# Kernel optimization log

Measured on AMD Instinct MI355X. Metric: run time of the kernel, lower is better.

The kernel has to match this reference:

```python
import jax, jax.numpy as jnp
import numpy as np

C, B, F, O, DK = 10, 8192, 256, 64, 5


def setup_inputs() -> dict:
    key = jax.random.key(0)
    ks = jax.random.split(key, 7)
    x = jax.random.normal(ks[0], (B, F), jnp.float32)
    y = jax.random.normal(ks[1], (B, C), jnp.float32)
    # kaiming-uniform-like init scales
    w_key = jax.random.normal(ks[2], (C, 1, 1, DK), jnp.float32) * 0.5
    w_query = jax.random.normal(ks[3], (C, 1, DK), jnp.float32) * 0.5
    w_value = jax.random.normal(ks[4], (C, 1, 1), jnp.float32) * 0.5
    weight = jax.random.normal(ks[5], (C, 1, F, O), jnp.float32) * (1.0 / np.sqrt(F))
    bias = jax.random.normal(ks[6], (C, 1, O), jnp.float32) * 0.1
    return {"x": x, "y": y, "w_key": w_key, "w_query": w_query,
            "w_value": w_value, "weight": weight, "bias": bias}


def reference(x, y, w_key, w_query, w_value, weight, bias):
    # x: [B,F] (first=True -> conceptually [1,B,F]); y: [B,C]
    yt = y.T                                             # [C,B]
    querys = yt[..., None] * w_query                     # [C,B,1]*[C,1,DK] -> [C,B,DK]
    # keys[c,b,f,k] = x[b,f] * w_key[c,k]; attn_scores[c,b,f] = sum_k keys*querys
    #              = x[b,f] * (w_key[c] . querys[c,b])  (rank-1 structure, fused)
    kq = jnp.einsum('ck,cbk->cb', w_key.reshape(w_key.shape[0], -1), querys)  # [C,B]
    # mean over batch dim, then softmax over features
    scores_avg = jnp.einsum('bf,cb->cf', x, kq) / x.shape[0]  # [C,F]
    sm = jax.nn.softmax(scores_avg, axis=-1)                  # [C,F]
    attn = sm / jnp.max(sm, axis=-1, keepdims=True)           # [C,F] max-normalized
    values = x[None, :, :] * w_value                          # [1,B,F]*[C,1,1] -> [C,B,F]
    weighted = values * attn[:, None, :]                      # [C,B,F]
    # (weighted[...,None,:] @ weight).squeeze() + bias -> [C,B,O]
    out = jnp.einsum('cbf,cfo->cbo', weighted, weight[:, 0]) + bias  # bias [C,1,O]
    return out
```

## Files before the change

### kernel.cpp

```cpp
#include <hip/hip_runtime.h>
#include <hip/hip_bf16.h>

#define C_ 10
#define B_ 8192
#define F_ 256
#define O_ 64
#define DK_ 5
#define NBLK1 256
#define NG2   16

typedef __attribute__((ext_vector_type(8))) short short8;
typedef __attribute__((ext_vector_type(4))) float floatx4;

static __device__ __forceinline__ unsigned short f2bf(float f) {
    union { float f; unsigned u; } v; v.f = f;
    unsigned r = v.u + 0x7fffu + ((v.u >> 16) & 1u);
    return (unsigned short)(r >> 16);
}

__global__ __launch_bounds__(256) void k1_reduce(const float* __restrict__ x,
                                                 const float* __restrict__ y,
                                                 float* __restrict__ G_part,
                                                 unsigned short* __restrict__ xb) {
    __shared__ float xl[32 * F_];
    __shared__ float yl[32 * C_];
    const int b0 = blockIdx.x * 32;
    const int t  = threadIdx.x;

    for (int i = t; i < 32 * C_; i += 256) yl[i] = y[b0 * C_ + i];

    const int r  = t >> 6;
    const int f4 = (t & 63) * 4;
#pragma unroll
    for (int j = 0; j < 8; ++j) {
        int row = r + 4 * j;
        float4 v = *(const float4*)(x + (size_t)(b0 + row) * F_ + f4);
        *(float4*)(xl + row * F_ + f4) = v;
        ushort4 s;
        s.x = f2bf(v.x); s.y = f2bf(v.y); s.z = f2bf(v.z); s.w = f2bf(v.w);
        *(ushort4*)(xb + (size_t)(b0 + row) * F_ + f4) = s;
    }
    __syncthreads();

    float acc[C_];
#pragma unroll
    for (int c = 0; c < C_; ++c) acc[c] = 0.f;

#pragma unroll 8
    for (int b = 0; b < 32; ++b) {
        float xv = xl[b * F_ + t];
#pragma unroll
        for (int c = 0; c < C_; ++c) acc[c] = fmaf(yl[b * C_ + c], xv, acc[c]);
    }

    float* gp = G_part + (size_t)blockIdx.x * C_ * F_ + t;
#pragma unroll
    for (int c = 0; c < C_; ++c) gp[c * F_] = acc[c];
}

__global__ __launch_bounds__(256) void k1b_reduce(const float* __restrict__ G_part,
                                                  float* __restrict__ G2) {
    const int c = (int)blockIdx.x >> 4;
    const int g = (int)blockIdx.x & 15;
    const int t = threadIdx.x;
    const float* gp = G_part + (size_t)(g * 16) * C_ * F_ + c * F_ + t;
    float a0 = 0.f, a1 = 0.f, a2 = 0.f, a3 = 0.f;
#pragma unroll
    for (int i = 0; i < 16; i += 4) {
        a0 += gp[(size_t)(i + 0) * C_ * F_];
        a1 += gp[(size_t)(i + 1) * C_ * F_];
        a2 += gp[(size_t)(i + 2) * C_ * F_];
        a3 += gp[(size_t)(i + 3) * C_ * F_];
    }
    G2[(size_t)g * C_ * F_ + c * F_ + t] = (a0 + a1) + (a2 + a3);
}

__global__ __launch_bounds__(256) void k2_wprep(const float* __restrict__ G2,
                                                const float* __restrict__ w_key,
                                                const float* __restrict__ w_query,
                                                const float* __restrict__ w_value,
                                                const float* __restrict__ weight,
                                                unsigned short* __restrict__ WT) {
    __shared__ float a2[F_];
    __shared__ float wred[4];
    const int c    = blockIdx.x >> 2;
    const int part = blockIdx.x & 3;
    const int t    = threadIdx.x;

    const float* gp = G2 + c * F_ + t;
    float g0 = 0.f, g1 = 0.f, g2 = 0.f, g3 = 0.f;
#pragma unroll
    for (int i = 0; i < NG2; i += 4) {
        g0 += gp[(size_t)(i + 0) * C_ * F_];
        g1 += gp[(size_t)(i + 1) * C_ * F_];
        g2 += gp[(size_t)(i + 2) * C_ * F_];
        g3 += gp[(size_t)(i + 3) * C_ * F_];
    }
    float g = (g0 + g1) + (g2 + g3);

    float s = 0.f;
#pragma unroll
    for (int k = 0; k < DK_; ++k) s += w_key[c * DK_ + k] * w_query[c * DK_ + k];

    float z = s * g * (1.0f / (float)B_);
    float m = z;
#pragma unroll
    for (int off = 32; off >= 1; off >>= 1) m = fmaxf(m, __shfl_xor(m, off));
    if ((t & 63) == 0) wred[t >> 6] = m;
    __syncthreads();
    float mm = fmaxf(fmaxf(wred[0], wred[1]), fmaxf(wred[2], wred[3]));
    a2[t] = expf(z - mm) * w_value[c];
    __syncthreads();

    const int o  = t & 63;
    const int fg = t >> 6;
    const float* wsrc = weight + (size_t)c * F_ * O_;
    char* wdst = (char*)(WT + (size_t)c * O_ * F_);
#pragma unroll
    for (int gi = 0; gi < 2; ++gi) {
        int f0 = part * 64 + fg * 16 + gi * 8;
        short8 v8;
#pragma unroll
        for (int e = 0; e < 8; ++e) {
            int f = f0 + e;
            v8[e] = (short)f2bf(wsrc[f * O_ + o] * a2[f]);
        }
        int byte = o * 512 + ((2 * f0) ^ ((o & 7) << 4));
        *(short8*)(wdst + byte) = v8;
    }
}

__global__ __launch_bounds__(256) void k3_mfma(const unsigned short* __restrict__ xb,
                                               const unsigned short* __restrict__ WT,
                                               const float* __restrict__ bias,
                                               float* __restrict__ out) {
    __shared__ unsigned short wt[O_ * F_];
    const int c  = blockIdx.y;
    const int b0 = blockIdx.x * 64;
    const int t  = threadIdx.x;
    const int w  = t >> 6;
    const int l  = t & 63;
    const int lr = l & 15;
    const int lg = l >> 4;

    const unsigned short* xrow = xb + (size_t)(b0 + w * 16 + lr) * F_;
    short8 a[8];
#pragma unroll
    for (int k0 = 0; k0 < 8; ++k0) a[k0] = *(const short8*)(xrow + k0 * 32 + lg * 8);

    {
        const short8* src = (const short8*)(WT + (size_t)c * O_ * F_);
        short8* dst = (short8*)wt;
#pragma unroll
        for (int j = 0; j < 8; ++j) dst[t + 256 * j] = src[t + 256 * j];
    }
    __syncthreads();

    floatx4 acc[4];
#pragma unroll
    for (int n = 0; n < 4; ++n) {
        float bo = bias[c * O_ + n * 16 + lr];
        acc[n] = (floatx4){bo, bo, bo, bo};
    }

#pragma unroll
    for (int k0 = 0; k0 < 8; ++k0) {
#pragma unroll
        for (int n = 0; n < 4; ++n) {
            int o = n * 16 + lr;
            int byte = o * 512 + ((k0 * 64 + lg * 16) ^ ((o & 7) << 4));
            short8 bf = *(const short8*)((const char*)wt + byte);
            acc[n] = __builtin_amdgcn_mfma_f32_16x16x32_bf16(a[k0], bf, acc[n], 0, 0, 0);
        }
    }

#pragma unroll
    for (int n = 0; n < 4; ++n) {
        int col = n * 16 + lr;
#pragma unroll
        for (int r = 0; r < 4; ++r) {
            int row = b0 + w * 16 + lg * 4 + r;
            out[((size_t)c * B_ + row) * O_ + col] = acc[n][r];
        }
    }
}

extern "C" void kernel_launch(void* const* d_in, const int* in_sizes, int n_in,
                              void* d_out, int out_size, void* d_ws, size_t ws_size,
                              hipStream_t stream) {
    const float* x       = (const float*)d_in[0];
    const float* y       = (const float*)d_in[1];
    const float* w_key   = (const float*)d_in[2];
    const float* w_query = (const float*)d_in[3];
    const float* w_value = (const float*)d_in[4];
    const float* weight  = (const float*)d_in[5];
    const float* bias    = (const float*)d_in[6];
    float* out = (float*)d_out;

    char* ws = (char*)d_ws;
    unsigned short* xb     = (unsigned short*)ws;
    unsigned short* WT     = (unsigned short*)(ws + (size_t)B_ * F_ * 2);
    float*          G_part = (float*)(ws + (size_t)B_ * F_ * 2 + C_ * O_ * F_ * 2);
    float*          G2     = G_part + (size_t)NBLK1 * C_ * F_;

    k1_reduce<<<NBLK1, 256, 0, stream>>>(x, y, G_part, xb);
    k1b_reduce<<<C_ * NG2, 256, 0, stream>>>(G_part, G2);
    k2_wprep<<<C_ * 4, 256, 0, stream>>>(G2, w_key, w_query, w_value, weight, WT);
    dim3 g3(B_ / 64, C_);
    k3_mfma<<<g3, 256, 0, stream>>>(xb, WT, bias, out);
}
```

Before: 27.72 us.

## Fuse weight preparation into the MFMA kernel, recomputing it per block

Removes the separate weight-prep kernel and its global bf16 WT buffer. Each GEMM block now reduces G2 itself, computes the softmax-derived scaling, scales and converts the 64KB fp32 weight slice, and writes it swizzled into shared memory. This saves one kernel launch and a global round trip. In exchange, all 1280 blocks redo the softmax and weight conversion and read the fp32 weights, which are twice the size of the bf16 copy they used to read.

```diff
diff --git a/kernel.cpp b/kernel.cpp
--- a/kernel.cpp
+++ b/kernel.cpp
@@ -75,66 +75,17 @@
     G2[(size_t)g * C_ * F_ + c * F_ + t] = (a0 + a1) + (a2 + a3);
 }
 
-__global__ __launch_bounds__(256) void k2_wprep(const float* __restrict__ G2,
+__global__ __launch_bounds__(256) void k3_fused(const unsigned short* __restrict__ xb,
+                                                const float* __restrict__ G2,
                                                 const float* __restrict__ w_key,
                                                 const float* __restrict__ w_query,
                                                 const float* __restrict__ w_value,
                                                 const float* __restrict__ weight,
-                                                unsigned short* __restrict__ WT) {
+                                                const float* __restrict__ bias,
+                                                float* __restrict__ out) {
+    __shared__ unsigned short wt[O_ * F_];
     __shared__ float a2[F_];
     __shared__ float wred[4];
-    const int c    = blockIdx.x >> 2;
-    const int part = blockIdx.x & 3;
-    const int t    = threadIdx.x;
-
-    const float* gp = G2 + c * F_ + t;
-    float g0 = 0.f, g1 = 0.f, g2 = 0.f, g3 = 0.f;
-#pragma unroll
-    for (int i = 0; i < NG2; i += 4) {
-        g0 += gp[(size_t)(i + 0) * C_ * F_];
-        g1 += gp[(size_t)(i + 1) * C_ * F_];
-        g2 += gp[(size_t)(i + 2) * C_ * F_];
-        g3 += gp[(size_t)(i + 3) * C_ * F_];
-    }
-    float g = (g0 + g1) + (g2 + g3);
-
-    float s = 0.f;
-#pragma unroll
-    for (int k = 0; k < DK_; ++k) s += w_key[c * DK_ + k] * w_query[c * DK_ + k];
-
-    float z = s * g * (1.0f / (float)B_);
-    float m = z;
-#pragma unroll
-    for (int off = 32; off >= 1; off >>= 1) m = fmaxf(m, __shfl_xor(m, off));
-    if ((t & 63) == 0) wred[t >> 6] = m;
-    __syncthreads();
-    float mm = fmaxf(fmaxf(wred[0], wred[1]), fmaxf(wred[2], wred[3]));
-    a2[t] = expf(z - mm) * w_value[c];
-    __syncthreads();
-
-    const int o  = t & 63;
-    const int fg = t >> 6;
-    const float* wsrc = weight + (size_t)c * F_ * O_;
-    char* wdst = (char*)(WT + (size_t)c * O_ * F_);
-#pragma unroll
-    for (int gi = 0; gi < 2; ++gi) {
-        int f0 = part * 64 + fg * 16 + gi * 8;
-        short8 v8;
-#pragma unroll
-        for (int e = 0; e < 8; ++e) {
-            int f = f0 + e;
-            v8[e] = (short)f2bf(wsrc[f * O_ + o] * a2[f]);
-        }
-        int byte = o * 512 + ((2 * f0) ^ ((o & 7) << 4));
-        *(short8*)(wdst + byte) = v8;
-    }
-}
-
-__global__ __launch_bounds__(256) void k3_mfma(const unsigned short* __restrict__ xb,
-                                               const unsigned short* __restrict__ WT,
-                                               const float* __restrict__ bias,
-                                               float* __restrict__ out) {
-    __shared__ unsigned short wt[O_ * F_];
     const int c  = blockIdx.y;
     const int b0 = blockIdx.x * 64;
     const int t  = threadIdx.x;
@@ -149,10 +100,46 @@
     for (int k0 = 0; k0 < 8; ++k0) a[k0] = *(const short8*)(xrow + k0 * 32 + lg * 8);
 
     {
-        const short8* src = (const short8*)(WT + (size_t)c * O_ * F_);
-        short8* dst = (short8*)wt;
+        const float* gp = G2 + c * F_ + t;
+        float g0 = 0.f, g1 = 0.f, g2 = 0.f, g3 = 0.f;
 #pragma unroll
-        for (int j = 0; j < 8; ++j) dst[t + 256 * j] = src[t + 256 * j];
+        for (int i = 0; i < NG2; i += 4) {
+            g0 += gp[(size_t)(i + 0) * C_ * F_];
+            g1 += gp[(size_t)(i + 1) * C_ * F_];
+            g2 += gp[(size_t)(i + 2) * C_ * F_];
+            g3 += gp[(size_t)(i + 3) * C_ * F_];
+        }
+        float g = (g0 + g1) + (g2 + g3);
+
+        float s = 0.f;
+#pragma unroll
+        for (int k = 0; k < DK_; ++k) s += w_key[c * DK_ + k] * w_query[c * DK_ + k];
+
+        float z = s * g * (1.0f / (float)B_);
+        float m = z;
+#pragma unroll
+        for (int off = 32; off >= 1; off >>= 1) m = fmaxf(m, __shfl_xor(m, off));
+        if ((t & 63) == 0) wred[t >> 6] = m;
+        __syncthreads();
+        float mm = fmaxf(fmaxf(wred[0], wred[1]), fmaxf(wred[2], wred[3]));
+        a2[t] = expf(z - mm) * w_value[c];
+        __syncthreads();
+    }
+
+    {
+        const float* wsrc = weight + (size_t)c * F_ * O_;
+#pragma unroll
+        for (int gi = 0; gi < 8; ++gi) {
+            int f0 = gi * 32 + w * 8;
+            short8 v8;
+#pragma unroll
+            for (int e = 0; e < 8; ++e) {
+                int f = f0 + e;
+                v8[e] = (short)f2bf(wsrc[f * O_ + l] * a2[f]);
+            }
+            int byte = l * 512 + ((2 * f0) ^ ((l & 7) << 4));
+            *(short8*)((char*)wt + byte) = v8;
+        }
     }
     __syncthreads();
 
@@ -199,13 +186,11 @@
 
     char* ws = (char*)d_ws;
     unsigned short* xb     = (unsigned short*)ws;
-    unsigned short* WT     = (unsigned short*)(ws + (size_t)B_ * F_ * 2);
-    float*          G_part = (float*)(ws + (size_t)B_ * F_ * 2 + C_ * O_ * F_ * 2);
+    float*          G_part = (float*)(ws + (size_t)B_ * F_ * 2);
     float*          G2     = G_part + (size_t)NBLK1 * C_ * F_;
 
     k1_reduce<<<NBLK1, 256, 0, stream>>>(x, y, G_part, xb);
     k1b_reduce<<<C_ * NG2, 256, 0, stream>>>(G_part, G2);
-    k2_wprep<<<C_ * 4, 256, 0, stream>>>(G2, w_key, w_query, w_value, weight, WT);
     dim3 g3(B_ / 64, C_);
-    k3_mfma<<<g3, 256, 0, stream>>>(xb, WT, bias, out);
+    k3_fused<<<g3, 256, 0, stream>>>(xb, G2, w_key, w_query, w_value, weight, bias, out);
 }
```

Measured after the change: 28.52 us. +2.9%, slower.
